# Performance work log

Measured on AMD Instinct MI355X. Metric: run time of the kernel, lower is better.

## Reference

```python
import jax, jax.numpy as jnp
import numpy as np

B, CIN, COUT, H, W, HEADS = 8, 128, 128, 256, 256, 32
CI = COUT // HEADS  # channels per head


def setup_inputs() -> dict:
    key = jax.random.key(0)
    ks = jax.random.split(key, 6)
    s_in = (2.0 / CIN) ** 0.5
    s_mid = (2.0 / COUT) ** 0.5
    return {
        "u": jax.random.normal(ks[0], (B, CIN, H, W), jnp.float32),
        "w_f1": jax.random.normal(ks[1], (COUT, CIN), jnp.float32) * s_in,
        "b_f1": jnp.zeros((COUT,), jnp.float32),
        # small flow weights -> small displacements (realistic warping)
        "w_f2": jax.random.normal(ks[2], (2 * HEADS, COUT), jnp.float32) * 0.02 * s_mid,
        "b_f2": jnp.zeros((2 * HEADS,), jnp.float32),
        "w_v": jax.random.normal(ks[3], (COUT, CIN), jnp.float32) * s_in,
        "b_v": jnp.zeros((COUT,), jnp.float32),
    }


def _conv1x1(x, w, b):
    # x: (B, Cin, H, W), w: (Cout, Cin) -> (B, Cout, H, W)
    return jnp.einsum('bchw,oc->bohw', x, w) + b[None, :, None, None]


def _periodic_bilinear(v, grid):
    """grid_sample, bilinear, align_corners=False, periodic in both H and W.
    Equivalent to custom_grid_sample2d with padding_modes=('periodic','periodic'):
    pixel coords are wrapped mod size and the (i+1) neighbor wraps to index 0
    (the torch code pads with the first row/col and samples with border mode).
    v: (N, C, H, W); grid: (N, H, W, 2) with [...,0]=x, [...,1]=y in [-1,1].
    """
    N, C, Hi, Wi = v.shape
    gx, gy = grid[..., 0], grid[..., 1]
    # unnormalize (align_corners=False) then wrap periodically
    px = jnp.mod(((gx + 1.0) * Wi - 1.0) * 0.5, Wi)
    py = jnp.mod(((gy + 1.0) * Hi - 1.0) * 0.5, Hi)
    x0 = jnp.floor(px)
    y0 = jnp.floor(py)
    wx = px - x0
    wy = py - y0
    x0i = jnp.clip(x0.astype(jnp.int32), 0, Wi - 1)
    y0i = jnp.clip(y0.astype(jnp.int32), 0, Hi - 1)
    x1i = jnp.mod(x0i + 1, Wi)
    y1i = jnp.mod(y0i + 1, Hi)
    vf = v.reshape(N, C, Hi * Wi)

    def gather(yi, xi):
        idx = (yi * Wi + xi).reshape(N, 1, Hi * Wi)
        return jnp.take_along_axis(vf, idx, axis=2).reshape(N, C, Hi, Wi)

    w00 = ((1.0 - wx) * (1.0 - wy))[:, None]
    w01 = (wx * (1.0 - wy))[:, None]
    w10 = ((1.0 - wx) * wy)[:, None]
    w11 = (wx * wy)[:, None]
    return (gather(y0i, x0i) * w00 + gather(y0i, x1i) * w01
            + gather(y1i, x0i) * w10 + gather(y1i, x1i) * w11)


def _base_grid(Hi, Wi):
    # create_grid: stack(meshgrid[::-1]) -> [...,0]=x (varies along W), [...,1]=y
    yy, xx = jnp.meshgrid(jnp.linspace(-1.0, 1.0, Hi),
                          jnp.linspace(-1.0, 1.0, Wi), indexing='ij')
    return jnp.stack([xx, yy], axis=-1)  # (H, W, 2)


def reference(u, w_f1, b_f1, w_f2, b_f2, w_v, b_v):
    Bq = u.shape[0]
    # flow_head: conv1x1 -> relu -> conv1x1
    hmid = jax.nn.relu(_conv1x1(u, w_f1, b_f1))
    flow = _conv1x1(hmid, w_f2, b_f2)          # (B, heads*2, H, W)
    value = _conv1x1(u, w_v, b_v)              # (B, Cout, H, W)
    # rearrange 'B (heads dir) H W -> (B heads) H W dir'
    flow = flow.reshape(Bq, HEADS, 2, H, W).transpose(0, 1, 3, 4, 2)
    flow = flow.reshape(Bq * HEADS, H, W, 2)
    grid = _base_grid(H, W)[None] + flow       # warp: x + delta(x)
    # rearrange 'B (heads C_i) H W -> (B heads) C_i H W'
    vh = value.reshape(Bq * HEADS, CI, H, W)
    out = _periodic_bilinear(vh, grid)
    # '(B heads) C_i H W -> B (heads C_i) H W'
    return out.reshape(Bq, COUT, H, W)
```

## Files before the change

kernel.cpp:

```cpp
#include <hip/hip_runtime.h>
#include <hip/hip_fp16.h>


typedef unsigned short u16;
typedef unsigned int   u32;
using short8   = __attribute__((ext_vector_type(8))) short;
using f32x4    = __attribute__((ext_vector_type(4))) float;
using ushort4v = __attribute__((ext_vector_type(4))) unsigned short;

#define HW     65536
#define NTILES 8192

__device__ __forceinline__ u16 f2h(float f) {
  return __half_as_ushort(__float2half(f));
}
__device__ __forceinline__ float h2f(u16 h) {
  return __half2float(__ushort_as_half(h));
}

__device__ __forceinline__ short8 frag_from_f32(const float* __restrict__ src) {
  float4 a = *(const float4*)src;
  float4 b = *(const float4*)(src + 4);
  short8 r;
  r[0] = (short)f2h(a.x); r[1] = (short)f2h(a.y);
  r[2] = (short)f2h(a.z); r[3] = (short)f2h(a.w);
  r[4] = (short)f2h(b.x); r[5] = (short)f2h(b.y);
  r[6] = (short)f2h(b.z); r[7] = (short)f2h(b.w);
  return r;
}

__global__ __launch_bounds__(256) void vf_kernel(
    const float* __restrict__ u,  const float* __restrict__ w1,
    const float* __restrict__ b1, const float* __restrict__ w2,
    const float* __restrict__ b2, const float* __restrict__ wv,
    const float* __restrict__ bv, u16* __restrict__ vout,
    u32* __restrict__ fout)
{
  __shared__ u16 t_lds[64 * 128];

  const int tid  = threadIdx.x;
  const int lane = tid & 63;
  const int w    = tid >> 6;
  const int m15  = lane & 15;
  const int q    = lane >> 4;

  short8 w1f[2][4], wvf[2][4], w2f[4];
#pragma unroll
  for (int nt = 0; nt < 2; ++nt)
#pragma unroll
    for (int kc = 0; kc < 4; ++kc) {
      const int row = w * 32 + nt * 16 + m15;
      w1f[nt][kc] = frag_from_f32(w1 + row * 128 + kc * 32 + q * 8);
      wvf[nt][kc] = frag_from_f32(wv + row * 128 + kc * 32 + q * 8);
    }
#pragma unroll
  for (int kc = 0; kc < 4; ++kc)
    w2f[kc] = frag_from_f32(w2 + (w * 16 + m15) * 128 + kc * 32 + q * 8);

  f32x4 vbias[2], hbias[2], fbias;
#pragma unroll
  for (int nt = 0; nt < 2; ++nt) {
    vbias[nt] = *(const f32x4*)(bv + w * 32 + nt * 16 + q * 4);
    hbias[nt] = *(const f32x4*)(b1 + w * 32 + nt * 16 + q * 4);
  }
  fbias = *(const f32x4*)(b2 + w * 16 + q * 4);

  for (int tile = blockIdx.x; tile < NTILES; tile += (int)gridDim.x) {
    const int gbase = tile << 6;
    const int b     = gbase >> 16;
    const int img   = gbase & 65535;
    const float* ub = u + ((size_t)b << 23) + img;

    {
      const int p  = tid & 63;
      const int cb = (tid >> 6) << 3;
#pragma unroll
      for (int pass = 0; pass < 4; ++pass) {
        int c0 = cb + pass * 32;
        float v0 = ub[(size_t)(c0 + 0) * HW + p];
        float v1 = ub[(size_t)(c0 + 1) * HW + p];
        float v2 = ub[(size_t)(c0 + 2) * HW + p];
        float v3 = ub[(size_t)(c0 + 3) * HW + p];
        float v4 = ub[(size_t)(c0 + 4) * HW + p];
        float v5 = ub[(size_t)(c0 + 5) * HW + p];
        float v6 = ub[(size_t)(c0 + 6) * HW + p];
        float v7 = ub[(size_t)(c0 + 7) * HW + p];
        uint4 pk;
        pk.x = (u32)f2h(v0) | ((u32)f2h(v1) << 16);
        pk.y = (u32)f2h(v2) | ((u32)f2h(v3) << 16);
        pk.z = (u32)f2h(v4) | ((u32)f2h(v5) << 16);
        pk.w = (u32)f2h(v6) | ((u32)f2h(v7) << 16);
        *(uint4*)((char*)t_lds + p * 256 + (((c0 >> 3) ^ (p & 15)) << 4)) = pk;
      }
    }
    __syncthreads();

    f32x4 zero = {0.f, 0.f, 0.f, 0.f};
    f32x4 hm[2][4], va[2][4];
#pragma unroll
    for (int nt = 0; nt < 2; ++nt)
#pragma unroll
      for (int pxb = 0; pxb < 4; ++pxb) { hm[nt][pxb] = zero; va[nt][pxb] = zero; }

#pragma unroll
    for (int kc = 0; kc < 4; ++kc) {
      short8 uf[4];
#pragma unroll
      for (int pxb = 0; pxb < 4; ++pxb)
        uf[pxb] = *(const short8*)((const char*)t_lds + (pxb * 16 + m15) * 256 +
                                   ((((kc << 2) + q) ^ m15) << 4));
#pragma unroll
      for (int pxb = 0; pxb < 4; ++pxb)
#pragma unroll
        for (int nt = 0; nt < 2; ++nt) {
          hm[nt][pxb] = __builtin_amdgcn_mfma_f32_16x16x32_f16(
              w1f[nt][kc], uf[pxb], hm[nt][pxb], 0, 0, 0);
          va[nt][pxb] = __builtin_amdgcn_mfma_f32_16x16x32_f16(
              wvf[nt][kc], uf[pxb], va[nt][pxb], 0, 0, 0);
        }
    }
    __syncthreads();

#pragma unroll
    for (int nt = 0; nt < 2; ++nt) {
      const int ch0   = w * 32 + nt * 16 + q * 4;
      const int chunk = ch0 >> 3;
      const int inner = (ch0 & 7) << 1;
#pragma unroll
      for (int pxb = 0; pxb < 4; ++pxb) {
        const int px = pxb * 16 + m15;
        float h0 = fmaxf(hm[nt][pxb][0] + hbias[nt][0], 0.f);
        float h1 = fmaxf(hm[nt][pxb][1] + hbias[nt][1], 0.f);
        float h2 = fmaxf(hm[nt][pxb][2] + hbias[nt][2], 0.f);
        float h3 = fmaxf(hm[nt][pxb][3] + hbias[nt][3], 0.f);
        uint2 pk;
        pk.x = (u32)f2h(h0) | ((u32)f2h(h1) << 16);
        pk.y = (u32)f2h(h2) | ((u32)f2h(h3) << 16);
        *(uint2*)((char*)t_lds + px * 256 + ((chunk ^ (px & 15)) << 4) + inner) = pk;
      }
    }

#pragma unroll
    for (int nt = 0; nt < 2; ++nt) {
      const int head = w * 8 + nt * 4 + q;
#pragma unroll
      for (int pxb = 0; pxb < 4; ++pxb) {
        f32x4 v = va[nt][pxb];
        uint2 pk;
        pk.x = (u32)f2h(v[0] + vbias[nt][0]) | ((u32)f2h(v[1] + vbias[nt][1]) << 16);
        pk.y = (u32)f2h(v[2] + vbias[nt][2]) | ((u32)f2h(v[3] + vbias[nt][3]) << 16);
        *(uint2*)(vout + ((((size_t)(b * 32 + head)) << 16) + img + pxb * 16 + m15) * 4) = pk;
      }
    }
    __syncthreads();

    f32x4 fl[4];
#pragma unroll
    for (int pxb = 0; pxb < 4; ++pxb) fl[pxb] = zero;
#pragma unroll
    for (int kc = 0; kc < 4; ++kc)
#pragma unroll
      for (int pxb = 0; pxb < 4; ++pxb) {
        short8 hf = *(const short8*)((const char*)t_lds + (pxb * 16 + m15) * 256 +
                                     ((((kc << 2) + q) ^ m15) << 4));
        fl[pxb] = __builtin_amdgcn_mfma_f32_16x16x32_f16(
            w2f[kc], hf, fl[pxb], 0, 0, 0);
      }

#pragma unroll
    for (int pxb = 0; pxb < 4; ++pxb) {
      f32x4 v = fl[pxb];
      const int h0 = w * 8 + q * 2;
      u32 pa = (u32)f2h(v[0] + fbias[0]) | ((u32)f2h(v[1] + fbias[1]) << 16);
      u32 pb = (u32)f2h(v[2] + fbias[2]) | ((u32)f2h(v[3] + fbias[3]) << 16);
      u32* fp = fout + (((size_t)(b * 32 + h0)) << 16) + img + pxb * 16 + m15;
      fp[0]  = pa;
      fp[HW] = pb;
    }
    __syncthreads();
  }
}

__global__ __launch_bounds__(256) void warp_kernel(
    const u16* __restrict__ value, const u32* __restrict__ flow,
    float* __restrict__ out)
{
  const int P  = blockIdx.x;
  const int l  = ((P & 7) << 13) | (P >> 3);
  const int gt = (l << 8) + (int)threadIdx.x;
  const int pix = gt & 65535;
  const int hb  = gt >> 16;

  u32 f    = flow[gt];
  float fx = h2f((u16)(f & 0xffffu));
  float fy = h2f((u16)(f >> 16));

  const int wq = pix & 255, hq = pix >> 8;
  float gx = -1.f + (2.f / 255.f) * (float)wq + fx;
  float gy = -1.f + (2.f / 255.f) * (float)hq + fy;
  float pxr = ((gx + 1.f) * 256.f - 1.f) * 0.5f;
  float pyr = ((gy + 1.f) * 256.f - 1.f) * 0.5f;
  float px = pxr - floorf(pxr * (1.f / 256.f)) * 256.f;
  float py = pyr - floorf(pyr * (1.f / 256.f)) * 256.f;
  if (px >= 256.f) px -= 256.f;
  if (py >= 256.f) py -= 256.f;
  if (px < 0.f) px = 0.f;
  if (py < 0.f) py = 0.f;

  float x0f = floorf(px), y0f = floorf(py);
  float wx = px - x0f, wy = py - y0f;
  int x0 = (int)x0f; if (x0 > 255) x0 = 255;
  int y0 = (int)y0f; if (y0 > 255) y0 = 255;
  int x1 = (x0 + 1) & 255;
  int y1 = (y0 + 1) & 255;

  float w00 = (1.f - wx) * (1.f - wy);
  float w01 = wx * (1.f - wy);
  float w10 = (1.f - wx) * wy;
  float w11 = wx * wy;

  const u16* vb = value + ((size_t)hb << 18);
  ushort4v t00 = *(const ushort4v*)(vb + ((y0 * 256 + x0) << 2));
  ushort4v t01 = *(const ushort4v*)(vb + ((y0 * 256 + x1) << 2));
  ushort4v t10 = *(const ushort4v*)(vb + ((y1 * 256 + x0) << 2));
  ushort4v t11 = *(const ushort4v*)(vb + ((y1 * 256 + x1) << 2));

  float* ob = out + ((size_t)hb << 18) + pix;
#pragma unroll
  for (int ci = 0; ci < 4; ++ci) {
    float r = w00 * h2f(t00[ci]) + w01 * h2f(t01[ci])
            + w10 * h2f(t10[ci]) + w11 * h2f(t11[ci]);
    ob[(size_t)ci << 16] = r;
  }
}

extern "C" void kernel_launch(void* const* d_in, const int* in_sizes, int n_in,
                              void* d_out, int out_size, void* d_ws, size_t ws_size,
                              hipStream_t stream) {
  const float* u  = (const float*)d_in[0];
  const float* w1 = (const float*)d_in[1];
  const float* b1 = (const float*)d_in[2];
  const float* w2 = (const float*)d_in[3];
  const float* b2 = (const float*)d_in[4];
  const float* wv = (const float*)d_in[5];
  const float* bv = (const float*)d_in[6];

  u16* value_ws = (u16*)d_ws;
  u32* flow_ws  = (u32*)((char*)d_ws + 134217728);
  float* out    = (float*)d_out;

  vf_kernel<<<dim3(512), dim3(256), 0, stream>>>(u, w1, b1, w2, b2, wv, bv,
                                                 value_ws, flow_ws);
  warp_kernel<<<dim3(65536), dim3(256), 0, stream>>>(value_ws, flow_ws, out);
}
```

Baseline: 664.1 us.

## Double-buffer input tiles in vf_kernel and process four rows per thread in warp

The conv kernel now prefetches the next tile's input into registers while the current tile's MFMAs run. It writes that data into a second LDS buffer at the end of each iteration and replaces __syncthreads with an lgkmcnt wait plus barrier. The warp kernel now has each thread handle four rows of one column, so each thread has 16 gathers in flight, and it writes output with nontemporal stores. The cost is 32 extra live registers in vf_kernel (launch bounds set to 2 blocks per SM), double the LDS, and a quarter as many warp blocks.

```diff
diff --git a/kernel.cpp b/kernel.cpp
--- a/kernel.cpp
+++ b/kernel.cpp
@@ -17,6 +17,12 @@
 __device__ __forceinline__ float h2f(u16 h) {
   return __half2float(__ushort_as_half(h));
 }
+
+#define BAR_LGKM() do {                                      \
+    asm volatile("s_waitcnt lgkmcnt(0)" ::: "memory");       \
+    __builtin_amdgcn_s_barrier();                            \
+    asm volatile("" ::: "memory");                           \
+  } while (0)
 
 __device__ __forceinline__ short8 frag_from_f32(const float* __restrict__ src) {
   float4 a = *(const float4*)src;
@@ -29,14 +35,44 @@
   return r;
 }
 
-__global__ __launch_bounds__(256) void vf_kernel(
+__device__ __forceinline__ void vf_load_tile(const float* __restrict__ u,
+                                             int tile, int tid,
+                                             float* __restrict__ r) {
+  const int gbase = tile << 6;
+  const float* ub = u + ((size_t)(gbase >> 16) << 23) + (gbase & 65535);
+  const int p  = tid & 63;
+  const int cb = (tid >> 6) << 3;
+#pragma unroll
+  for (int pass = 0; pass < 4; ++pass)
+#pragma unroll
+    for (int j = 0; j < 8; ++j)
+      r[pass * 8 + j] = ub[(size_t)(cb + pass * 32 + j) * HW + p];
+}
+
+__device__ __forceinline__ void vf_write_tile(u16* __restrict__ buf, int tid,
+                                              const float* __restrict__ r) {
+  const int p  = tid & 63;
+  const int cb = (tid >> 6) << 3;
+#pragma unroll
+  for (int pass = 0; pass < 4; ++pass) {
+    int c0 = cb + pass * 32;
+    uint4 pk;
+    pk.x = (u32)f2h(r[pass * 8 + 0]) | ((u32)f2h(r[pass * 8 + 1]) << 16);
+    pk.y = (u32)f2h(r[pass * 8 + 2]) | ((u32)f2h(r[pass * 8 + 3]) << 16);
+    pk.z = (u32)f2h(r[pass * 8 + 4]) | ((u32)f2h(r[pass * 8 + 5]) << 16);
+    pk.w = (u32)f2h(r[pass * 8 + 6]) | ((u32)f2h(r[pass * 8 + 7]) << 16);
+    *(uint4*)((char*)buf + p * 256 + (((c0 >> 3) ^ (p & 15)) << 4)) = pk;
+  }
+}
+
+__global__ __launch_bounds__(256, 2) void vf_kernel(
     const float* __restrict__ u,  const float* __restrict__ w1,
     const float* __restrict__ b1, const float* __restrict__ w2,
     const float* __restrict__ b2, const float* __restrict__ wv,
     const float* __restrict__ bv, u16* __restrict__ vout,
     u32* __restrict__ fout)
 {
-  __shared__ u16 t_lds[64 * 128];
+  __shared__ u16 t_lds[2][64 * 128];
 
   const int tid  = threadIdx.x;
   const int lane = tid & 63;
@@ -65,35 +101,23 @@
   }
   fbias = *(const f32x4*)(b2 + w * 16 + q * 4);
 
-  for (int tile = blockIdx.x; tile < NTILES; tile += (int)gridDim.x) {
+  const int step = (int)gridDim.x;
+  int tile = blockIdx.x;
+  float sreg[32];
+
+  vf_load_tile(u, tile, tid, sreg);
+  vf_write_tile(t_lds[0], tid, sreg);
+  BAR_LGKM();
+
+  int cur = 0;
+  for (; tile < NTILES; ) {
     const int gbase = tile << 6;
     const int b     = gbase >> 16;
     const int img   = gbase & 65535;
-    const float* ub = u + ((size_t)b << 23) + img;
-
-    {
-      const int p  = tid & 63;
-      const int cb = (tid >> 6) << 3;
-#pragma unroll
-      for (int pass = 0; pass < 4; ++pass) {
-        int c0 = cb + pass * 32;
-        float v0 = ub[(size_t)(c0 + 0) * HW + p];
-        float v1 = ub[(size_t)(c0 + 1) * HW + p];
-        float v2 = ub[(size_t)(c0 + 2) * HW + p];
-        float v3 = ub[(size_t)(c0 + 3) * HW + p];
-        float v4 = ub[(size_t)(c0 + 4) * HW + p];
-        float v5 = ub[(size_t)(c0 + 5) * HW + p];
-        float v6 = ub[(size_t)(c0 + 6) * HW + p];
-        float v7 = ub[(size_t)(c0 + 7) * HW + p];
-        uint4 pk;
-        pk.x = (u32)f2h(v0) | ((u32)f2h(v1) << 16);
-        pk.y = (u32)f2h(v2) | ((u32)f2h(v3) << 16);
-        pk.z = (u32)f2h(v4) | ((u32)f2h(v5) << 16);
-        pk.w = (u32)f2h(v6) | ((u32)f2h(v7) << 16);
-        *(uint4*)((char*)t_lds + p * 256 + (((c0 >> 3) ^ (p & 15)) << 4)) = pk;
-      }
-    }
-    __syncthreads();
+    const int nxt   = tile + step;
+    const bool have_next = (nxt < NTILES);
+
+    if (have_next) vf_load_tile(u, nxt, tid, sreg);
 
     f32x4 zero = {0.f, 0.f, 0.f, 0.f};
     f32x4 hm[2][4], va[2][4];
@@ -107,7 +131,8 @@
       short8 uf[4];
 #pragma unroll
       for (int pxb = 0; pxb < 4; ++pxb)
-        uf[pxb] = *(const short8*)((const char*)t_lds + (pxb * 16 + m15) * 256 +
+        uf[pxb] = *(const short8*)((const char*)t_lds[cur] +
+                                   (pxb * 16 + m15) * 256 +
                                    ((((kc << 2) + q) ^ m15) << 4));
 #pragma unroll
       for (int pxb = 0; pxb < 4; ++pxb)
@@ -119,7 +144,7 @@
               wvf[nt][kc], uf[pxb], va[nt][pxb], 0, 0, 0);
         }
     }
-    __syncthreads();
+    BAR_LGKM();
 
 #pragma unroll
     for (int nt = 0; nt < 2; ++nt) {
@@ -136,7 +161,8 @@
         uint2 pk;
         pk.x = (u32)f2h(h0) | ((u32)f2h(h1) << 16);
         pk.y = (u32)f2h(h2) | ((u32)f2h(h3) << 16);
-        *(uint2*)((char*)t_lds + px * 256 + ((chunk ^ (px & 15)) << 4) + inner) = pk;
+        *(uint2*)((char*)t_lds[cur] + px * 256 + ((chunk ^ (px & 15)) << 4) +
+                  inner) = pk;
       }
     }
 
@@ -149,10 +175,11 @@
         uint2 pk;
         pk.x = (u32)f2h(v[0] + vbias[nt][0]) | ((u32)f2h(v[1] + vbias[nt][1]) << 16);
         pk.y = (u32)f2h(v[2] + vbias[nt][2]) | ((u32)f2h(v[3] + vbias[nt][3]) << 16);
-        *(uint2*)(vout + ((((size_t)(b * 32 + head)) << 16) + img + pxb * 16 + m15) * 4) = pk;
+        *(uint2*)(vout + ((((size_t)(b * 32 + head)) << 16) + img +
+                          pxb * 16 + m15) * 4) = pk;
       }
     }
-    __syncthreads();
+    BAR_LGKM();
 
     f32x4 fl[4];
 #pragma unroll
@@ -161,7 +188,8 @@
     for (int kc = 0; kc < 4; ++kc)
 #pragma unroll
       for (int pxb = 0; pxb < 4; ++pxb) {
-        short8 hf = *(const short8*)((const char*)t_lds + (pxb * 16 + m15) * 256 +
+        short8 hf = *(const short8*)((const char*)t_lds[cur] +
+                                     (pxb * 16 + m15) * 256 +
                                      ((((kc << 2) + q) ^ m15) << 4));
         fl[pxb] = __builtin_amdgcn_mfma_f32_16x16x32_f16(
             w2f[kc], hf, fl[pxb], 0, 0, 0);
@@ -177,7 +205,11 @@
       fp[0]  = pa;
       fp[HW] = pb;
     }
-    __syncthreads();
+
+    if (have_next) vf_write_tile(t_lds[cur ^ 1], tid, sreg);
+    BAR_LGKM();
+    cur ^= 1;
+    tile = nxt;
   }
 }
 
@@ -185,53 +217,61 @@
     const u16* __restrict__ value, const u32* __restrict__ flow,
     float* __restrict__ out)
 {
-  const int P  = blockIdx.x;
-  const int l  = ((P & 7) << 13) | (P >> 3);
-  const int gt = (l << 8) + (int)threadIdx.x;
-  const int pix = gt & 65535;
-  const int hb  = gt >> 16;
-
-  u32 f    = flow[gt];
-  float fx = h2f((u16)(f & 0xffffu));
-  float fy = h2f((u16)(f >> 16));
-
-  const int wq = pix & 255, hq = pix >> 8;
-  float gx = -1.f + (2.f / 255.f) * (float)wq + fx;
-  float gy = -1.f + (2.f / 255.f) * (float)hq + fy;
-  float pxr = ((gx + 1.f) * 256.f - 1.f) * 0.5f;
-  float pyr = ((gy + 1.f) * 256.f - 1.f) * 0.5f;
-  float px = pxr - floorf(pxr * (1.f / 256.f)) * 256.f;
-  float py = pyr - floorf(pyr * (1.f / 256.f)) * 256.f;
-  if (px >= 256.f) px -= 256.f;
-  if (py >= 256.f) py -= 256.f;
-  if (px < 0.f) px = 0.f;
-  if (py < 0.f) py = 0.f;
-
-  float x0f = floorf(px), y0f = floorf(py);
-  float wx = px - x0f, wy = py - y0f;
-  int x0 = (int)x0f; if (x0 > 255) x0 = 255;
-  int y0 = (int)y0f; if (y0 > 255) y0 = 255;
-  int x1 = (x0 + 1) & 255;
-  int y1 = (y0 + 1) & 255;
-
-  float w00 = (1.f - wx) * (1.f - wy);
-  float w01 = wx * (1.f - wy);
-  float w10 = (1.f - wx) * wy;
-  float w11 = wx * wy;
+  const int P   = blockIdx.x;
+  const int L   = ((P & 7) << 11) | (P >> 3);
+  const int hb  = L >> 6;
+  const int g   = L & 63;
+  const int col = threadIdx.x;
 
   const u16* vb = value + ((size_t)hb << 18);
-  ushort4v t00 = *(const ushort4v*)(vb + ((y0 * 256 + x0) << 2));
-  ushort4v t01 = *(const ushort4v*)(vb + ((y0 * 256 + x1) << 2));
-  ushort4v t10 = *(const ushort4v*)(vb + ((y1 * 256 + x0) << 2));
-  ushort4v t11 = *(const ushort4v*)(vb + ((y1 * 256 + x1) << 2));
-
-  float* ob = out + ((size_t)hb << 18) + pix;
-#pragma unroll
-  for (int ci = 0; ci < 4; ++ci) {
-    float r = w00 * h2f(t00[ci]) + w01 * h2f(t01[ci])
-            + w10 * h2f(t10[ci]) + w11 * h2f(t11[ci]);
-    ob[(size_t)ci << 16] = r;
-  }
+  const u32* fp = flow + ((size_t)hb << 16) + (g << 10) + col;
+
+  u32 f[4];
+#pragma unroll
+  for (int r = 0; r < 4; ++r) f[r] = fp[r << 8];
+
+  float w00[4], w01[4], w10[4], w11[4];
+  ushort4v t00[4], t01[4], t10[4], t11[4];
+#pragma unroll
+  for (int r = 0; r < 4; ++r) {
+    float fx = h2f((u16)(f[r] & 0xffffu));
+    float fy = h2f((u16)(f[r] >> 16));
+    const int hq = (g << 2) + r;
+    float gx = -1.f + (2.f / 255.f) * (float)col + fx;
+    float gy = -1.f + (2.f / 255.f) * (float)hq + fy;
+    float pxr = ((gx + 1.f) * 256.f - 1.f) * 0.5f;
+    float pyr = ((gy + 1.f) * 256.f - 1.f) * 0.5f;
+    float px = pxr - floorf(pxr * (1.f / 256.f)) * 256.f;
+    float py = pyr - floorf(pyr * (1.f / 256.f)) * 256.f;
+    if (px >= 256.f) px -= 256.f;
+    if (py >= 256.f) py -= 256.f;
+    if (px < 0.f) px = 0.f;
+    if (py < 0.f) py = 0.f;
+    float x0f = floorf(px), y0f = floorf(py);
+    float wx = px - x0f, wy = py - y0f;
+    int x0 = (int)x0f; if (x0 > 255) x0 = 255;
+    int y0 = (int)y0f; if (y0 > 255) y0 = 255;
+    int x1 = (x0 + 1) & 255;
+    int y1 = (y0 + 1) & 255;
+    w00[r] = (1.f - wx) * (1.f - wy);
+    w01[r] = wx * (1.f - wy);
+    w10[r] = (1.f - wx) * wy;
+    w11[r] = wx * wy;
+    t00[r] = *(const ushort4v*)(vb + ((y0 * 256 + x0) << 2));
+    t01[r] = *(const ushort4v*)(vb + ((y0 * 256 + x1) << 2));
+    t10[r] = *(const ushort4v*)(vb + ((y1 * 256 + x0) << 2));
+    t11[r] = *(const ushort4v*)(vb + ((y1 * 256 + x1) << 2));
+  }
+
+  float* ob = out + ((size_t)hb << 18) + (g << 10) + col;
+#pragma unroll
+  for (int r = 0; r < 4; ++r)
+#pragma unroll
+    for (int ci = 0; ci < 4; ++ci) {
+      float res = w00[r] * h2f(t00[r][ci]) + w01[r] * h2f(t01[r][ci])
+                + w10[r] * h2f(t10[r][ci]) + w11[r] * h2f(t11[r][ci]);
+      __builtin_nontemporal_store(res, ob + (r << 8) + ((size_t)ci << 16));
+    }
 }
 
 extern "C" void kernel_launch(void* const* d_in, const int* in_sizes, int n_in,
@@ -251,5 +291,5 @@
 
   vf_kernel<<<dim3(512), dim3(256), 0, stream>>>(u, w1, b1, w2, b2, wv, bv,
                                                  value_ws, flow_ws);
-  warp_kernel<<<dim3(65536), dim3(256), 0, stream>>>(value_ws, flow_ws, out);
-}
+  warp_kernel<<<dim3(16384), dim3(256), 0, stream>>>(value_ws, flow_ws, out);
+}
```

Result: slower. 766.7 us (+15.5%).
